# Kernel optimization log

Measured on AMD Instinct MI355X. Metric: run time of the kernel, lower is better.

Reference implementation:

```python
import jax, jax.numpy as jnp
import numpy as np
from jax import lax

NUM_CHANNELS = 32
PROT_SECTION = 4
PROT_SIZE = NUM_CHANNELS * PROT_SECTION  # 128
BATCH = 128
SEQ_LEN = 8194


def setup_inputs() -> dict:
    key = jax.random.key(0)
    ks = jax.random.split(key, 6)
    input_seq = jax.random.randint(ks[0], (BATCH, SEQ_LEN), 0, 26)
    emb = jax.random.normal(ks[1], (26, 5), dtype=jnp.float32)
    conv_w = jax.random.normal(ks[2], (NUM_CHANNELS, 5, 3), dtype=jnp.float32) * 0.1
    conv_b = jnp.zeros((NUM_CHANNELS,), dtype=jnp.float32)
    W_a = jax.random.normal(ks[3], (PROT_SIZE, PROT_SIZE), dtype=jnp.float32) / np.sqrt(PROT_SIZE)
    v_a = jax.random.normal(ks[4], (PROT_SIZE,), dtype=jnp.float32)
    return {"input_seq": input_seq, "emb": emb, "conv_w": conv_w,
            "conv_b": conv_b, "W_a": W_a, "v_a": v_a}


def reference(input_seq, emb, conv_w, conv_b, W_a, v_a):
    # Embedding lookup: [B, L, 5] -> [B, 5, L]
    x = emb[input_seq].transpose(0, 2, 1)
    # Conv1d(5 -> C, k=3, valid) + bias + ReLU  (dropout is identity in eval)
    y = lax.conv_general_dilated(x, conv_w, window_strides=(1,), padding='VALID',
                                 dimension_numbers=('NCH', 'OIH', 'NCH'))
    y = jax.nn.relu(y + conv_b[None, :, None])  # [B, C, L-2]
    B, C, PL = y.shape
    S = PROT_SECTION
    new_L = PL // S
    rem = PL % S
    head = rem // 2
    tail = PL - (rem - head)
    y = y[:, :, head:tail].reshape(B, C * S, new_L)  # [B, D, N], D = C*S
    # Batched self-attention pooling (original loops over batch in Python)
    # energies[b, n] = v_a @ tanh(W_a @ H_b)
    e = jnp.einsum('d,bdn->bn', v_a, jnp.tanh(jnp.einsum('de,ben->bdn', W_a, y)))
    w = jax.nn.softmax(e, axis=-1)  # stable softmax; same math as unstable F.softmax
    ctx = jnp.einsum('bn,bdn->bd', w, y)  # [B, D]
    return ctx
```

## Files before the change

kernel.cpp:

```cpp
#include <hip/hip_runtime.h>

#define LSEQ 8194

typedef _Float16 f16x8 __attribute__((ext_vector_type(8)));
typedef _Float16 f16x2 __attribute__((ext_vector_type(2)));
typedef __attribute__((ext_vector_type(4))) float f32x4;

static __device__ __forceinline__ float tanh_fast(float x){
    float p = __expf(2.0f * x);
    float r = __builtin_amdgcn_rcpf(1.0f + p);
    return 1.0f - 2.0f * r;
}
static __device__ __forceinline__ unsigned h3relu(unsigned a, unsigned b, unsigned c){
    union { f16x2 h; unsigned u; } x, y, z, r;
    x.u = a; y.u = b; z.u = c;
    f16x2 s = x.h + y.h + z.h;
    f16x2 zero = { (_Float16)0.0f, (_Float16)0.0f };
    r.h = __builtin_elementwise_max(s, zero);
    return r.u;
}
static __device__ __forceinline__ unsigned hpack(float a, float b){
    union { f16x2 h; unsigned u; } pk;
    pk.h = (f16x2){ (_Float16)a, (_Float16)b };
    return pk.u;
}

__global__ __launch_bounds__(512, 6) void k_fused(
        const int* __restrict__ seq, const float* __restrict__ emb,
        const float* __restrict__ cw, const float* __restrict__ cb,
        const float* __restrict__ Wa, const float* __restrict__ va,
        float* __restrict__ part, float* __restrict__ stats)
{
    __shared__ __align__(16) unsigned wahL[8192];
    __shared__ __align__(16) unsigned tblH[1560];
    __shared__ unsigned short seqw16[4][260];
    __shared__ __align__(16) float vaL[128];

    int tid = threadIdx.x;
    int b   = blockIdx.y;
    int x   = blockIdx.x;
    int n0  = x * 256;

    for (int i = tid; i < 8192; i += 512){
        float2 t = ((const float2*)Wa)[i];
        unsigned byteoff = ((unsigned)i << 2) ^ ((((unsigned)i >> 6) & 7u) << 4);
        *(unsigned*)((char*)wahL + byteoff) = hpack(t.x, t.y);
    }
    if (tid < 128) vaL[tid] = va[tid];
    const int* sb = seq + (size_t)b * LSEQ;
    for (int i = tid; i < 4*258; i += 512){
        int s = i / 258, off = i - s*258;
        seqw16[s][off] = (unsigned short)(sb[s*2048 + n0 + off] * 80);
    }
    for (int gid = tid; gid < 1248; gid += 512){
        int k = gid / 416;
        int rem = gid - k*416;
        int l = rem >> 4;
        int cp = rem & 15;
        int c0 = cp*2;
        float v0 = 0.f, v1 = 0.f;
        #pragma unroll
        for (int i = 0; i < 5; i++){
            float e = emb[l*5 + i];
            v0 += cw[(c0*5 + i)*3 + k] * e;
            v1 += cw[((c0+1)*5 + i)*3 + k] * e;
        }
        if (k == 2){ v0 += cb[c0]; v1 += cb[c0+1]; }
        tblH[k*520 + l*20 + (cp & 3)*4 + (cp >> 2)] = hpack(v0, v1);
    }
    __syncthreads();

    int w = tid >> 6, lane = tid & 63;
    int m = lane & 15, q = lane >> 4;
    const char* tb0 = (const char*)tblH + q*16;
    const char* tb1 = tb0 + 2080;
    const char* tb2 = tb1 + 2080;

    float accp[32];
    #pragma unroll
    for (int j = 0; j < 32; j++) accp[j] = 0.f;
    float Mw = -3e38f, Sw = 0.f;

    #pragma unroll
    for (int it = 0; it < 2; it++){
        int base = w*32 + it*16 + m;
        uint4 vfr[4];
        {
            unsigned V[4][4];
            #pragma unroll
            for (int s = 0; s < 4; s++){
                unsigned oa = seqw16[s][base];
                unsigned ob = seqw16[s][base+1];
                unsigned oc = seqw16[s][base+2];
                uint4 t0 = *(const uint4*)(tb0 + oa);
                uint4 t1 = *(const uint4*)(tb1 + ob);
                uint4 t2 = *(const uint4*)(tb2 + oc);
                V[s][0] = h3relu(t0.x, t1.x, t2.x);
                V[s][1] = h3relu(t0.y, t1.y, t2.y);
                V[s][2] = h3relu(t0.z, t1.z, t2.z);
                V[s][3] = h3relu(t0.w, t1.w, t2.w);
            }
            #pragma unroll
            for (int ki = 0; ki < 4; ki++){
                uint4 o;
                o.x = __builtin_amdgcn_perm(V[1][ki], V[0][ki], 0x05040100u);
                o.y = __builtin_amdgcn_perm(V[3][ki], V[2][ki], 0x05040100u);
                o.z = __builtin_amdgcn_perm(V[1][ki], V[0][ki], 0x07060302u);
                o.w = __builtin_amdgcn_perm(V[3][ki], V[2][ki], 0x07060302u);
                vfr[ki] = o;
            }
        }

        float ep = 0.f;
        #pragma unroll
        for (int dt = 0; dt < 8; dt++){
            f32x4 acc = (f32x4){0.f, 0.f, 0.f, 0.f};
            #pragma unroll
            for (int ki = 0; ki < 4; ki++){
                unsigned abyte = (unsigned)((dt*16 + m)*256 + ki*64 + q*16)
                               ^ (((unsigned)(m & 7)) << 4);
                union { uint4 u; f16x8 f; } af, bf;
                af.u = *(const uint4*)((const char*)wahL + abyte);
                bf.u = vfr[ki];
                acc = __builtin_amdgcn_mfma_f32_16x16x32_f16(af.f, bf.f, acc, 0, 0, 0);
            }
            const f32x4 vg = *(const f32x4*)&vaL[dt*16 + q*4];
            ep += vg[0] * tanh_fast(acc[0]);
            ep += vg[1] * tanh_fast(acc[1]);
            ep += vg[2] * tanh_fast(acc[2]);
            ep += vg[3] * tanh_fast(acc[3]);
        }
        ep += __shfl_xor(ep, 16);
        ep += __shfl_xor(ep, 32);

        float msub = ep;
        #pragma unroll
        for (int off = 8; off >= 1; off >>= 1)
            msub = fmaxf(msub, __shfl_xor(msub, off));
        float Mnew = fmaxf(Mw, msub);
        float alpha = __expf(Mw - Mnew);
        float wrl = __expf(ep - Mnew);
        float ssub = wrl;
        #pragma unroll
        for (int off = 8; off >= 1; off >>= 1) ssub += __shfl_xor(ssub, off);
        Sw = alpha * Sw + ssub;
        Mw = Mnew;

        #pragma unroll
        for (int ki = 0; ki < 4; ki++){
            union { uint4 u; f16x2 h[4]; } vv; vv.u = vfr[ki];
            accp[ki*8 + 0] = alpha * accp[ki*8 + 0] + wrl * (float)vv.h[0][0];
            accp[ki*8 + 1] = alpha * accp[ki*8 + 1] + wrl * (float)vv.h[0][1];
            accp[ki*8 + 2] = alpha * accp[ki*8 + 2] + wrl * (float)vv.h[1][0];
            accp[ki*8 + 3] = alpha * accp[ki*8 + 3] + wrl * (float)vv.h[1][1];
            accp[ki*8 + 4] = alpha * accp[ki*8 + 4] + wrl * (float)vv.h[2][0];
            accp[ki*8 + 5] = alpha * accp[ki*8 + 5] + wrl * (float)vv.h[2][1];
            accp[ki*8 + 6] = alpha * accp[ki*8 + 6] + wrl * (float)vv.h[3][0];
            accp[ki*8 + 7] = alpha * accp[ki*8 + 7] + wrl * (float)vv.h[3][1];
        }
    }

    #pragma unroll
    for (int j = 0; j < 32; j++){
        accp[j] += __shfl_xor(accp[j], 1);
        accp[j] += __shfl_xor(accp[j], 2);
        accp[j] += __shfl_xor(accp[j], 4);
        accp[j] += __shfl_xor(accp[j], 8);
    }
    size_t chunk = ((size_t)b*8 + x)*8 + w;
    if (m == 0){
        float* pd = part + chunk*128;
        #pragma unroll
        for (int ki = 0; ki < 4; ki++){
            float4 lo = { accp[ki*8+0], accp[ki*8+1], accp[ki*8+2], accp[ki*8+3] };
            float4 hi = { accp[ki*8+4], accp[ki*8+5], accp[ki*8+6], accp[ki*8+7] };
            *(float4*)(pd + ki*32 + q*8)     = lo;
            *(float4*)(pd + ki*32 + q*8 + 4) = hi;
        }
    }
    if (lane == 0){
        stats[chunk*2    ] = Mw;
        stats[chunk*2 + 1] = Sw;
    }
}

__global__ __launch_bounds__(128) void kb2_finish(const float* __restrict__ part,
        const float* __restrict__ stats, float* __restrict__ out)
{
    int b = blockIdx.x, d = threadIdx.x;
    const float* st = stats + (size_t)b*128;
    float M = -3e38f;
    #pragma unroll 8
    for (int c = 0; c < 64; c++) M = fmaxf(M, st[c*2]);
    const float* p = part + (size_t)b*64*128 + d;
    float S = 0.f, s = 0.f;
    #pragma unroll 4
    for (int c = 0; c < 64; c++){
        float f = __expf(st[c*2] - M);
        S += st[c*2+1] * f;
        s += p[c*128] * f;
    }
    float inv = 1.0f / S;
    out[b*128 + d] = s * inv;
}

extern "C" void kernel_launch(void* const* d_in, const int* in_sizes, int n_in,
                              void* d_out, int out_size, void* d_ws, size_t ws_size,
                              hipStream_t stream)
{
    const int*   seq = (const int*)d_in[0];
    const float* emb = (const float*)d_in[1];
    const float* cw  = (const float*)d_in[2];
    const float* cb  = (const float*)d_in[3];
    const float* Wa  = (const float*)d_in[4];
    const float* va  = (const float*)d_in[5];
    float* out = (float*)d_out;

    char* wsb = (char*)d_ws;
    float* part  = (float*)wsb;
    float* stats = (float*)(wsb + (8<<20));

    k_fused   <<<dim3(8,128), 512, 0, stream>>>(seq, emb, cw, cb, Wa, va, part, stats);
    kb2_finish<<<128,         128, 0, stream>>>(part, stats, out);
}
```

Baseline: 108.8 us.

## Double per-block sequence coverage and batch MFMA A-fragment loads across four tiles

Each block now covers 512 positions per section instead of 256, so the grid halves and the per-block cost of staging W_a, the lookup table and v_a into shared memory is spread over twice the work. The MFMA loop now loads four A fragments and keeps four independent accumulators, which exposes more instruction-level parallelism. The finish kernel reduces 32 partial chunks per batch row instead of 64. The trade-off is more registers (the launch-bounds occupancy hint drops from 6 to 2), fewer blocks to hide latency, and a position loop that is no longer unrolled.

```diff
diff --git a/kernel.cpp b/kernel.cpp
--- a/kernel.cpp
+++ b/kernel.cpp
@@ -25,7 +25,7 @@
     return pk.u;
 }
 
-__global__ __launch_bounds__(512, 6) void k_fused(
+__global__ __launch_bounds__(512, 2) void k_fused(
         const int* __restrict__ seq, const float* __restrict__ emb,
         const float* __restrict__ cw, const float* __restrict__ cb,
         const float* __restrict__ Wa, const float* __restrict__ va,
@@ -33,13 +33,13 @@
 {
     __shared__ __align__(16) unsigned wahL[8192];
     __shared__ __align__(16) unsigned tblH[1560];
-    __shared__ unsigned short seqw16[4][260];
+    __shared__ unsigned short seqw16[4][520];
     __shared__ __align__(16) float vaL[128];
 
     int tid = threadIdx.x;
     int b   = blockIdx.y;
     int x   = blockIdx.x;
-    int n0  = x * 256;
+    int n0  = x * 512;
 
     for (int i = tid; i < 8192; i += 512){
         float2 t = ((const float2*)Wa)[i];
@@ -48,9 +48,10 @@
     }
     if (tid < 128) vaL[tid] = va[tid];
     const int* sb = seq + (size_t)b * LSEQ;
-    for (int i = tid; i < 4*258; i += 512){
-        int s = i / 258, off = i - s*258;
-        seqw16[s][off] = (unsigned short)(sb[s*2048 + n0 + off] * 80);
+    for (int i = tid; i < 4*520; i += 512){
+        int s = i / 520, off = i - s*520;
+        if (off < 514)
+            seqw16[s][off] = (unsigned short)(sb[s*2048 + n0 + off] * 80);
     }
     for (int gid = tid; gid < 1248; gid += 512){
         int k = gid / 416;
@@ -81,9 +82,8 @@
     for (int j = 0; j < 32; j++) accp[j] = 0.f;
     float Mw = -3e38f, Sw = 0.f;
 
-    #pragma unroll
-    for (int it = 0; it < 2; it++){
-        int base = w*32 + it*16 + m;
+    for (int it = 0; it < 4; it++){
+        int base = w*64 + it*16 + m;
         uint4 vfr[4];
         {
             unsigned V[4][4];
@@ -113,22 +113,36 @@
 
         float ep = 0.f;
         #pragma unroll
-        for (int dt = 0; dt < 8; dt++){
-            f32x4 acc = (f32x4){0.f, 0.f, 0.f, 0.f};
+        for (int h = 0; h < 2; h++){
+            f32x4 acc[4];
+            #pragma unroll
+            for (int dd = 0; dd < 4; dd++) acc[dd] = (f32x4){0.f, 0.f, 0.f, 0.f};
             #pragma unroll
             for (int ki = 0; ki < 4; ki++){
-                unsigned abyte = (unsigned)((dt*16 + m)*256 + ki*64 + q*16)
-                               ^ (((unsigned)(m & 7)) << 4);
-                union { uint4 u; f16x8 f; } af, bf;
-                af.u = *(const uint4*)((const char*)wahL + abyte);
-                bf.u = vfr[ki];
-                acc = __builtin_amdgcn_mfma_f32_16x16x32_f16(af.f, bf.f, acc, 0, 0, 0);
-            }
-            const f32x4 vg = *(const f32x4*)&vaL[dt*16 + q*4];
-            ep += vg[0] * tanh_fast(acc[0]);
-            ep += vg[1] * tanh_fast(acc[1]);
-            ep += vg[2] * tanh_fast(acc[2]);
-            ep += vg[3] * tanh_fast(acc[3]);
+                uint4 af[4];
+                #pragma unroll
+                for (int dd = 0; dd < 4; dd++){
+                    int dt = h*4 + dd;
+                    unsigned abyte = (unsigned)((dt*16 + m)*256 + ki*64 + q*16)
+                                   ^ (((unsigned)(m & 7)) << 4);
+                    af[dd] = *(const uint4*)((const char*)wahL + abyte);
+                }
+                union { uint4 u; f16x8 f; } bf; bf.u = vfr[ki];
+                #pragma unroll
+                for (int dd = 0; dd < 4; dd++){
+                    union { uint4 u; f16x8 f; } a; a.u = af[dd];
+                    acc[dd] = __builtin_amdgcn_mfma_f32_16x16x32_f16(a.f, bf.f, acc[dd], 0, 0, 0);
+                }
+            }
+            #pragma unroll
+            for (int dd = 0; dd < 4; dd++){
+                int dt = h*4 + dd;
+                const f32x4 vg = *(const f32x4*)&vaL[dt*16 + q*4];
+                ep += vg[0] * tanh_fast(acc[dd][0]);
+                ep += vg[1] * tanh_fast(acc[dd][1]);
+                ep += vg[2] * tanh_fast(acc[dd][2]);
+                ep += vg[3] * tanh_fast(acc[dd][3]);
+            }
         }
         ep += __shfl_xor(ep, 16);
         ep += __shfl_xor(ep, 32);
@@ -167,7 +181,7 @@
         accp[j] += __shfl_xor(accp[j], 4);
         accp[j] += __shfl_xor(accp[j], 8);
     }
-    size_t chunk = ((size_t)b*8 + x)*8 + w;
+    size_t chunk = ((size_t)b*4 + x)*8 + w;
     if (m == 0){
         float* pd = part + chunk*128;
         #pragma unroll
@@ -188,14 +202,14 @@
         const float* __restrict__ stats, float* __restrict__ out)
 {
     int b = blockIdx.x, d = threadIdx.x;
-    const float* st = stats + (size_t)b*128;
+    const float* st = stats + (size_t)b*64;
     float M = -3e38f;
     #pragma unroll 8
-    for (int c = 0; c < 64; c++) M = fmaxf(M, st[c*2]);
-    const float* p = part + (size_t)b*64*128 + d;
+    for (int c = 0; c < 32; c++) M = fmaxf(M, st[c*2]);
+    const float* p = part + (size_t)b*32*128 + d;
     float S = 0.f, s = 0.f;
     #pragma unroll 4
-    for (int c = 0; c < 64; c++){
+    for (int c = 0; c < 32; c++){
         float f = __expf(st[c*2] - M);
         S += st[c*2+1] * f;
         s += p[c*128] * f;
@@ -218,8 +232,8 @@
 
     char* wsb = (char*)d_ws;
     float* part  = (float*)wsb;
-    float* stats = (float*)(wsb + (8<<20));
-
-    k_fused   <<<dim3(8,128), 512, 0, stream>>>(seq, emb, cw, cb, Wa, va, part, stats);
+    float* stats = (float*)(wsb + (4<<20));
+
+    k_fused   <<<dim3(4,128), 512, 0, stream>>>(seq, emb, cw, cb, Wa, va, part, stats);
     kb2_finish<<<128,         128, 0, stream>>>(part, stats, out);
 }
```

Result: no change. 108.6 us (-0.2%).
